# Optimization experiments

Measured on AMD Instinct MI355X. Metric: run time of the kernel, lower is better.

The kernel has to match this reference:

```python
import jax, jax.numpy as jnp
import numpy as np

INPUT_CHANNELS = 3

def setup_inputs() -> dict:
    key = jax.random.key(0)
    kx, ky = jax.random.split(key)
    x = jax.random.normal(kx, (8, 4096, 3), dtype=jnp.float32)
    y = jax.random.normal(ky, (8, 4096, 3), dtype=jnp.float32)
    return {"x": x, "y": y}

def reference(x, y):
    # Match torch: truncate both clouds to common num_points and input_channels.
    num_points = min(x.shape[1], y.shape[1])
    x = x[:, :num_points, :INPUT_CHANNELS]
    y = y[:, :num_points, :INPUT_CHANNELS]
    # pdist[b, i, j] = ||x_i||^2 + ||y_j||^2 - 2 x_i . y_j  (squared Euclidean)
    x2 = jnp.sum(x * x, axis=-1)          # [B, N]
    y2 = jnp.sum(y * y, axis=-1)          # [B, N]
    zz = jnp.einsum('bic,bjc->bij', x, y) # [B, N, N]
    pdist = x2[:, :, None] + y2[:, None, :] - 2.0 * zz
    # min over i (dim 1): nearest x for each y; min over j (dim 2): nearest y for each x
    loss = jnp.mean(jnp.min(pdist, axis=1)) + jnp.mean(jnp.min(pdist, axis=2))
    return loss * 0.005
```

## Files before the change

kernel.cpp:

```cpp
#include <hip/hip_runtime.h>

#define NPTS 4096
#define NB   8
#define TOT  (2 * NB * NPTS)

typedef __attribute__((ext_vector_type(8)))  short          bf16x8;
typedef __attribute__((ext_vector_type(8)))  unsigned short u16x8;
typedef __attribute__((ext_vector_type(16))) float          f32x16;

__device__ __forceinline__ unsigned short bf16_rne(float f) {
    unsigned u = __float_as_uint(f);
    u += 0x7FFFu + ((u >> 16) & 1u);
    return (unsigned short)(u >> 16);
}
__device__ __forceinline__ float bf16_f(unsigned short s) {
    return __uint_as_float(((unsigned)s) << 16);
}


__global__ __launch_bounds__(256) void prep_b(
    const float* __restrict__ x, const float* __restrict__ y,
    unsigned short* __restrict__ Bform, unsigned* __restrict__ smax,
    float* __restrict__ out)
{
    int i   = blockIdx.x * 256 + threadIdx.x;
    int cid = i >> 12;
    int p   = i & 4095;
    const float* src = (cid < 8) ? x + ((size_t)cid * NPTS + p) * 3
                                 : y + ((size_t)(cid - 8) * NPTS + p) * 3;
    float c0 = src[0], c1 = src[1], c2 = src[2];
    float h  = -0.5f * (c0 * c0 + c1 * c1 + c2 * c2);

    unsigned short h0 = bf16_rne(c0), h1 = bf16_rne(c1), h2 = bf16_rne(c2);
    unsigned short l0 = bf16_rne(c0 - bf16_f(h0));
    unsigned short l1 = bf16_rne(c1 - bf16_f(h1));
    unsigned short l2 = bf16_rne(c2 - bf16_f(h2));
    unsigned short hh = bf16_rne(h);
    unsigned short hl = bf16_rne(h - bf16_f(hh));

    u16x8 blo, bhi;
    blo[0]=h0; blo[1]=h1; blo[2]=h2; blo[3]=h0; blo[4]=h1; blo[5]=h2; blo[6]=l0; blo[7]=l1;
    bhi[0]=l2; bhi[1]=hh; bhi[2]=hl; bhi[3]=0; bhi[4]=0; bhi[5]=0; bhi[6]=0; bhi[7]=0;

    int u = p >> 5, pos = p & 31;
    size_t base = ((size_t)cid << 17) + (size_t)u * 1024 + (size_t)pos * 16;
    *(u16x8*)((char*)Bform + base)       = blo;
    *(u16x8*)((char*)Bform + base + 512) = bhi;

    smax[i] = 0u;
    if (i == 0) *out = 0.f;
}

__global__ __launch_bounds__(256, 2) void chamfer_mfma(
    const float* __restrict__ x, const float* __restrict__ y,
    const unsigned short* __restrict__ Bform,
    unsigned* __restrict__ smax)
{
    __shared__ float buf[4][64][33];

    const int bid  = blockIdx.x;
    const int dirb = bid >> 5;
    const int sub  = bid & 31;
    const int iblk = sub >> 2;
    const int jq   = sub & 3;

    const int tid = threadIdx.x;
    const int w   = tid >> 6;
    const int l   = tid & 63;
    const int g   = l >> 5;
    const int pos = l & 31;

    const float* Araw = (dirb < 8) ? x + (size_t)dirb * NPTS * 3
                                   : y + (size_t)(dirb - 8) * NPTS * 3;
    const char* Bbase = (const char*)Bform + ((size_t)(dirb ^ 8) << 17);

    const int it0 = iblk * 16 + w * 4;
    bf16x8 afr[4];
    #pragma unroll
    for (int t = 0; t < 4; ++t) {
        const float* ap = Araw + (size_t)((it0 + t) * 32 + pos) * 3;
        float c0 = ap[0], c1 = ap[1], c2 = ap[2];
        unsigned short h0 = bf16_rne(c0), h1 = bf16_rne(c1), h2 = bf16_rne(c2);
        unsigned short l0 = bf16_rne(c0 - bf16_f(h0));
        unsigned short l1 = bf16_rne(c1 - bf16_f(h1));
        unsigned short l2 = bf16_rne(c2 - bf16_f(h2));
        const short ONE = (short)0x3F80;
        bf16x8 alo, ahi;
        alo[0]=(short)h0; alo[1]=(short)h1; alo[2]=(short)h2; alo[3]=(short)l0;
        alo[4]=(short)l1; alo[5]=(short)l2; alo[6]=(short)h0; alo[7]=(short)h1;
        ahi[0]=(short)h2; ahi[1]=ONE; ahi[2]=ONE; ahi[3]=0;
        ahi[4]=0; ahi[5]=0; ahi[6]=0; ahi[7]=0;
        #pragma unroll
        for (int e = 0; e < 8; ++e) afr[t][e] = g ? ahi[e] : alo[e];
    }

    f32x16 zc;
    #pragma unroll
    for (int r = 0; r < 16; ++r) zc[r] = 0.f;

    f32x16 run[4];
    #pragma unroll
    for (int t = 0; t < 4; ++t)
        #pragma unroll
        for (int r = 0; r < 16; ++r) run[t][r] = -3.0e38f;

    f32x16 p0, p1;
    #pragma unroll
    for (int r = 0; r < 16; ++r) { p0[r] = -3.0e38f; p1[r] = -3.0e38f; }

    const char* Bq = Bbase + (size_t)(jq * 32) * 1024
                           + (size_t)g * 512 + (size_t)pos * 16;

    bf16x8 cb0 = *(const bf16x8*)(Bq);
    bf16x8 cb1 = *(const bf16x8*)(Bq + 1024);
    bf16x8 cb2 = *(const bf16x8*)(Bq + 2048);
    bf16x8 cb3 = *(const bf16x8*)(Bq + 3072);

#define STAGE(T, B0, B1, RP)                                                    \
    {                                                                           \
        f32x16 d0 = __builtin_amdgcn_mfma_f32_32x32x16_bf16(afr[T], B0, zc, 0, 0, 0); \
        f32x16 d1 = __builtin_amdgcn_mfma_f32_32x32x16_bf16(afr[T], B1, zc, 0, 0, 0); \
        _Pragma("unroll")                                                       \
        for (int r = 0; r < 16; ++r)                                            \
            run[RP][r] = fmaxf(fmaxf(p0[r], p1[r]), run[RP][r]);                \
        p0 = d0; p1 = d1;                                                       \
    }

    #pragma unroll 1
    for (int j = 0; j < 32; j += 4) {
        bf16x8 nb0, nb1, nb2, nb3;
        if (j < 28) {
            const char* Bn = Bq + (size_t)(j + 4) * 1024;
            nb0 = *(const bf16x8*)(Bn);
            nb1 = *(const bf16x8*)(Bn + 1024);
            nb2 = *(const bf16x8*)(Bn + 2048);
            nb3 = *(const bf16x8*)(Bn + 3072);
        }
        STAGE(0, cb0, cb1, 3)
        STAGE(1, cb0, cb1, 0)
        STAGE(2, cb0, cb1, 1)
        STAGE(3, cb0, cb1, 2)
        STAGE(0, cb2, cb3, 3)
        STAGE(1, cb2, cb3, 0)
        STAGE(2, cb2, cb3, 1)
        STAGE(3, cb2, cb3, 2)
        if (j < 28) { cb0 = nb0; cb1 = nb1; cb2 = nb2; cb3 = nb3; }
    }
#undef STAGE

    #pragma unroll
    for (int r = 0; r < 16; ++r)
        run[3][r] = fmaxf(fmaxf(p0[r], p1[r]), run[3][r]);

    #pragma unroll
    for (int ph = 0; ph < 2; ++ph) {
        if (ph) __syncthreads();
        #pragma unroll
        for (int tl = 0; tl < 2; ++tl) {
            const int t = 2 * ph + tl;
            #pragma unroll
            for (int r = 0; r < 16; ++r) {
                int rowin = (r & 3) + 8 * (r >> 2) + 4 * g;
                buf[w][tl * 32 + rowin][pos] = run[t][r];
            }
        }
        __syncthreads();

        float m = buf[w][l][0];
        #pragma unroll
        for (int k = 1; k < 32; ++k) m = fmaxf(m, buf[w][l][k]);
        int idx = dirb * 4096 + iblk * 512 + w * 128 + 2 * ph * 32 + l;
        unsigned bits = __float_as_uint(m);
        unsigned mu = (bits & 0x80000000u) ? ~bits : (bits | 0x80000000u);
        atomicMax(&smax[idx], mu);
    }
}

__global__ __launch_bounds__(256) void reduce_kernel(
    const unsigned* __restrict__ smax,
    const float* __restrict__ x, const float* __restrict__ y,
    float* __restrict__ out)
{
    const int stride = 64 * 256;
    int tid = blockIdx.x * 256 + threadIdx.x;
    float s = 0.f;
    for (int k = tid; k < TOT; k += stride) {
        unsigned u = smax[k];
        unsigned bits = (u & 0x80000000u) ? (u & 0x7FFFFFFFu) : ~u;
        int cid = k >> 12, p = k & 4095;
        const float* ap = (cid < 8) ? x + ((size_t)cid * NPTS + p) * 3
                                    : y + ((size_t)(cid - 8) * NPTS + p) * 3;
        float a0 = ap[0], a1 = ap[1], a2 = ap[2];
        s += __uint_as_float(bits) - 0.5f * (a0 * a0 + a1 * a1 + a2 * a2);
    }

    #pragma unroll
    for (int off = 32; off > 0; off >>= 1)
        s += __shfl_down(s, off);

    __shared__ float redb[4];
    const int lane = threadIdx.x & 63, wave = threadIdx.x >> 6;
    if (lane == 0) redb[wave] = s;
    __syncthreads();
    if (threadIdx.x == 0) {
        float t = redb[0] + redb[1] + redb[2] + redb[3];
        atomicAdd(out, t * (-2.0f * 0.005f / 32768.f));
    }
}

extern "C" void kernel_launch(void* const* d_in, const int* in_sizes, int n_in,
                              void* d_out, int out_size, void* d_ws, size_t ws_size,
                              hipStream_t stream) {
    const float* x = (const float*)d_in[0];
    const float* y = (const float*)d_in[1];
    float* out = (float*)d_out;

    unsigned short* Bform = (unsigned short*)d_ws;
    unsigned*       smax  = (unsigned*)((char*)d_ws + (2u << 20));

    prep_b<<<dim3(TOT / 256), dim3(256), 0, stream>>>(x, y, Bform, smax, out);
    chamfer_mfma<<<dim3(512), dim3(256), 0, stream>>>(x, y, Bform, smax);
    reduce_kernel<<<dim3(64), dim3(256), 0, stream>>>(smax, x, y, out);
}
```

Before: 69.54 us.

## Fuse final reduction into MFMA kernel via last-block counter

Removes the separate reduce kernel. The squared-norm term is now summed inside prep_b with a block reduction and atomicAdd, and the min-sum over smax is done by the last-finishing chamfer block, found with an atomic counter and threadfence. A hipMemsetAsync zeroes the output. This saves a kernel launch and a re-read of x/y, but the final 32K-element reduction now runs serially in one block using atomic reads, and a memset call is added.

Result: slower. 162.9 us (+134.3%).

```diff
diff --git a/kernel.cpp b/kernel.cpp
--- a/kernel.cpp
+++ b/kernel.cpp
@@ -3,6 +3,7 @@
 #define NPTS 4096
 #define NB   8
 #define TOT  (2 * NB * NPTS)
+#define SCALE (-2.0f * 0.005f / 32768.f)
 
 typedef __attribute__((ext_vector_type(8)))  short          bf16x8;
 typedef __attribute__((ext_vector_type(8)))  unsigned short u16x8;
@@ -21,7 +22,7 @@
 __global__ __launch_bounds__(256) void prep_b(
     const float* __restrict__ x, const float* __restrict__ y,
     unsigned short* __restrict__ Bform, unsigned* __restrict__ smax,
-    float* __restrict__ out)
+    unsigned* __restrict__ counter, float* __restrict__ out)
 {
     int i   = blockIdx.x * 256 + threadIdx.x;
     int cid = i >> 12;
@@ -48,13 +49,25 @@
     *(u16x8*)((char*)Bform + base + 512) = bhi;
 
     smax[i] = 0u;
-    if (i == 0) *out = 0.f;
+    if (i == 0) *counter = 0u;
+
+    float s = h;
+    #pragma unroll
+    for (int off = 32; off > 0; off >>= 1)
+        s += __shfl_down(s, off);
+    __shared__ float redb[4];
+    const int lane = threadIdx.x & 63, wv = threadIdx.x >> 6;
+    if (lane == 0) redb[wv] = s;
+    __syncthreads();
+    if (threadIdx.x == 0)
+        atomicAdd(out, (redb[0] + redb[1] + redb[2] + redb[3]) * SCALE);
 }
 
 __global__ __launch_bounds__(256, 2) void chamfer_mfma(
     const float* __restrict__ x, const float* __restrict__ y,
     const unsigned short* __restrict__ Bform,
-    unsigned* __restrict__ smax)
+    unsigned* __restrict__ smax, unsigned* __restrict__ counter,
+    float* __restrict__ out)
 {
     __shared__ float buf[4][64][33];
 
@@ -174,37 +187,27 @@
         unsigned mu = (bits & 0x80000000u) ? ~bits : (bits | 0x80000000u);
         atomicMax(&smax[idx], mu);
     }
-}
-
-__global__ __launch_bounds__(256) void reduce_kernel(
-    const unsigned* __restrict__ smax,
-    const float* __restrict__ x, const float* __restrict__ y,
-    float* __restrict__ out)
-{
-    const int stride = 64 * 256;
-    int tid = blockIdx.x * 256 + threadIdx.x;
-    float s = 0.f;
-    for (int k = tid; k < TOT; k += stride) {
-        unsigned u = smax[k];
-        unsigned bits = (u & 0x80000000u) ? (u & 0x7FFFFFFFu) : ~u;
-        int cid = k >> 12, p = k & 4095;
-        const float* ap = (cid < 8) ? x + ((size_t)cid * NPTS + p) * 3
-                                    : y + ((size_t)(cid - 8) * NPTS + p) * 3;
-        float a0 = ap[0], a1 = ap[1], a2 = ap[2];
-        s += __uint_as_float(bits) - 0.5f * (a0 * a0 + a1 * a1 + a2 * a2);
-    }
-
-    #pragma unroll
-    for (int off = 32; off > 0; off >>= 1)
-        s += __shfl_down(s, off);
-
-    __shared__ float redb[4];
-    const int lane = threadIdx.x & 63, wave = threadIdx.x >> 6;
-    if (lane == 0) redb[wave] = s;
+
+    __threadfence();
+    __shared__ unsigned lastflag;
+    if (tid == 0) lastflag = atomicAdd(counter, 1u);
     __syncthreads();
-    if (threadIdx.x == 0) {
-        float t = redb[0] + redb[1] + redb[2] + redb[3];
-        atomicAdd(out, t * (-2.0f * 0.005f / 32768.f));
+    if (lastflag == 511u) {
+        float s = 0.f;
+        for (int k = tid; k < TOT; k += 256) {
+            unsigned uv = atomicMax(&smax[k], 0u);
+            unsigned bits = (uv & 0x80000000u) ? (uv & 0x7FFFFFFFu) : ~uv;
+            s += __uint_as_float(bits);
+        }
+        #pragma unroll
+        for (int off = 32; off > 0; off >>= 1)
+            s += __shfl_down(s, off);
+        __syncthreads();
+        float* redb = &buf[0][0][0];
+        if (l == 0) redb[w] = s;
+        __syncthreads();
+        if (tid == 0)
+            atomicAdd(out, (redb[0] + redb[1] + redb[2] + redb[3]) * SCALE);
     }
 }
 
@@ -215,10 +218,11 @@
     const float* y = (const float*)d_in[1];
     float* out = (float*)d_out;
 
-    unsigned short* Bform = (unsigned short*)d_ws;
-    unsigned*       smax  = (unsigned*)((char*)d_ws + (2u << 20));
-
-    prep_b<<<dim3(TOT / 256), dim3(256), 0, stream>>>(x, y, Bform, smax, out);
-    chamfer_mfma<<<dim3(512), dim3(256), 0, stream>>>(x, y, Bform, smax);
-    reduce_kernel<<<dim3(64), dim3(256), 0, stream>>>(smax, x, y, out);
-}
+    unsigned short* Bform   = (unsigned short*)d_ws;
+    unsigned*       smax    = (unsigned*)((char*)d_ws + (2u << 20));
+    unsigned*       counter = (unsigned*)((char*)d_ws + (2u << 20) + (256u << 10));
+
+    hipMemsetAsync(out, 0, sizeof(float), stream);
+    prep_b<<<dim3(TOT / 256), dim3(256), 0, stream>>>(x, y, Bform, smax, counter, out);
+    chamfer_mfma<<<dim3(512), dim3(256), 0, stream>>>(x, y, Bform, smax, counter, out);
+}
```
